# Kernel optimization log

Measured on AMD Instinct MI355X. Metric: run time of the kernel, lower is better.

## Reference

```python
import jax, jax.numpy as jnp
import numpy as np
from jax import lax

N_SRC = 2
K_BASES = 8
N_ITER = 5
NMF_EPS = 1e-20
IP_EPS = 1e-20


def setup_inputs() -> dict:
    key = jax.random.key(0)
    kx, kt, kv = jax.random.split(key, 3)
    M, J, I = 2, 2048, 1025
    X = jax.random.normal(kx, (M, J, I, 2), dtype=jnp.float32)
    T0 = jax.random.uniform(kt, (I, K_BASES, N_SRC), dtype=jnp.float32,
                            minval=1e-08, maxval=1.0)
    V0 = jax.random.uniform(kv, (K_BASES, J, N_SRC), dtype=jnp.float32,
                            minval=1e-08, maxval=1.0)
    return {"X": X, "T0": T0, "V0": V0}


def _nmf_update(Tn, Vn, Yn, eps):
    # Tn: (I,K), Vn: (K,J), Yn: (I,J) complex
    Rn = Tn @ Vn
    magR = jnp.abs(Rn)
    YdR = jnp.abs(Yn) ** 2 / (magR ** 2 + eps)   # |Y|^2 / R^2
    Rd = 1.0 / (magR + eps)
    Tn = Tn * jnp.sqrt((YdR @ Vn.T) / (Rd @ Vn.T + eps))
    Rn = Tn @ Vn
    Rd2 = 1.0 / (jnp.abs(Rn) + eps)
    Vn = Vn * jnp.sqrt((Tn.T @ YdR) / (Tn.T @ Rd2 + eps))
    return Tn, Vn, Tn @ Vn


def _ilrma(X, T0, V0):
    M, J, I, _ = X.shape
    N = N_SRC
    # view_as_complex(X.permute(2,0,1,3)) -> (I, M, J) complex
    Xc = (X[..., 0] + 1j * X[..., 1]).astype(jnp.complex64).transpose(2, 0, 1)
    eye_M = jnp.eye(M, dtype=jnp.complex64)
    W0 = jnp.broadcast_to(jnp.eye(N, M, dtype=jnp.complex64), (I, N, M))
    Y0 = jnp.einsum('inm,imj->inj', W0, Xc)

    def one_iter(carry, _):
        W, T, V, Y = carry
        for n in range(N):  # N=2, structurally distinct small loop
            Tn, Vn, Rn = _nmf_update(T[:, :, n], V[:, :, n], Y[:, n, :], NMF_EPS)
            T = T.at[:, :, n].set(Tn)
            V = V.at[:, :, n].set(Vn)
            # batched per-frequency-bin IP update (vectorizes torch's loop over i)
            inv_Rn = 1.0 / (Rn + IP_EPS)                      # (I,J)
            Xw = Xc * jnp.sqrt(inv_Rn)[:, None, :]            # (I,M,J)
            D = jnp.einsum('imj,ikj->imk', Xw, Xw.conj()) / J  # (I,M,M)
            Dreg = D + IP_EPS * eye_M
            A = jnp.einsum('inm,imk->ink', W, Dreg)           # (I,N,M), N==M
            e_n = eye_M[:, n]                                  # (M,)
            b = jnp.linalg.solve(A, jnp.broadcast_to(e_n, (I, M))[..., None])[..., 0]  # (I,M)
            Db = jnp.einsum('imk,ik->im', Dreg, b)
            denom = jnp.sqrt(jnp.real(jnp.einsum('im,im->i', b.conj(), Db)) + IP_EPS)
            W = W.at[:, n, :].set((b / denom[:, None]).conj())
        Y = jnp.einsum('inm,imj->inj', W, Xc)
        return (W, T, V, Y), None

    (W, T, V, Y), _ = lax.scan(one_iter, (W0, T0, V0, Y0), None, length=N_ITER)
    out = Y.transpose(1, 2, 0)                 # (N, J, I)
    return jnp.stack([out.real, out.imag], axis=-1)  # view_as_real -> (N,J,I,2)


def reference(X, T0, V0):
    return _ilrma(X, T0, V0)
```

## Files before the change

kernel.cpp:

```cpp
#include <hip/hip_runtime.h>

#define I_DIM 1025
#define J_DIM 2048
#define K_B 8
#define IC 33
#define EPSF 1e-20f


__device__ __forceinline__ int rev4i(int x) {
  return ((x & 1) << 3) | ((x & 2) << 1) | ((x & 4) >> 1) | ((x & 8) >> 3);
}
__device__ __forceinline__ int rev3i(int x) {
  return ((x & 1) << 2) | (x & 2) | ((x & 4) >> 2);
}

__device__ __forceinline__ void foldReduce16(float* vals, int lane) {
  #pragma unroll
  for (int step = 0; step < 4; ++step) {
    const int nv = 8 >> step;
    const int bit = (lane >> step) & 1;
    #pragma unroll
    for (int q = 0; q < nv; ++q) {
      float a = vals[q], b = vals[q + nv];
      float send = bit ? a : b;
      float keep = bit ? b : a;
      vals[q] = keep + __shfl_xor(send, 1 << step);
    }
  }
  vals[0] += __shfl_xor(vals[0], 16);
  vals[0] += __shfl_xor(vals[0], 32);
}

__device__ __forceinline__ void foldReduce8(float* vals, int lane) {
  #pragma unroll
  for (int step = 0; step < 3; ++step) {
    const int nv = 4 >> step;
    const int bit = (lane >> step) & 1;
    #pragma unroll
    for (int q = 0; q < nv; ++q) {
      float a = vals[q], b = vals[q + nv];
      float send = bit ? a : b;
      float keep = bit ? b : a;
      vals[q] = keep + __shfl_xor(send, 1 << step);
    }
  }
  vals[0] += __shfl_xor(vals[0], 8);
  vals[0] += __shfl_xor(vals[0], 16);
  vals[0] += __shfl_xor(vals[0], 32);
}

__device__ __forceinline__ float2 cmul(float2 a, float2 b) {
  return make_float2(a.x*b.x - a.y*b.y, a.x*b.y + a.y*b.x);
}
__device__ __forceinline__ float2 cadd(float2 a, float2 b) {
  return make_float2(a.x + b.x, a.y + b.y);
}
__device__ __forceinline__ float2 csub(float2 a, float2 b) {
  return make_float2(a.x - b.x, a.y - b.y);
}
__device__ __forceinline__ float2 cdiv(float2 a, float2 b) {
  float s = 1.0f / (b.x*b.x + b.y*b.y);
  return make_float2((a.x*b.x + a.y*b.y)*s, (a.y*b.x - a.x*b.y)*s);
}

__global__ __launch_bounds__(256) void k_tr_init(
    const float* __restrict__ X, float4* __restrict__ Xq,
    const float* __restrict__ T0, const float* __restrict__ V0,
    float* __restrict__ T, float* __restrict__ V, float* __restrict__ W)
{
  const int tx = threadIdx.x, ty = threadIdx.y;
  const int lt = ty * 32 + tx;
  const int bid = blockIdx.y * 33 + blockIdx.x;
  int t = bid * 256 + lt;
  if (t < 2 * K_B * J_DIM) {
    int n = t >> 14;
    int r = t & 16383;
    int j = r >> 3, k = r & 7;
    V[t] = V0[(k * J_DIM + j) * 2 + n];
  }
  if (t < 2 * I_DIM * K_B) {
    int n = t / (I_DIM * K_B);
    int r = t % (I_DIM * K_B);
    int i = r / K_B, k = r % K_B;
    T[t] = T0[(i * K_B + k) * 2 + n];
  }
  if (t < I_DIM * 8) {
    int u = t & 7;
    int c = u & 1, m = (u >> 1) & 1, n = u >> 2;
    W[t] = (n == m && c == 0) ? 1.0f : 0.0f;
  }
  __shared__ float t0r[32][33], t0i[32][33], t1r[32][33], t1i[32][33];
  const int i0 = blockIdx.x * 32, j0 = blockIdx.y * 32;
  const float2* __restrict__ X2 = (const float2*)X;
  #pragma unroll
  for (int jj = 0; jj < 4; ++jj) {
    int jl = ty + jj * 8;
    int i = i0 + tx;
    if (i < I_DIM) {
      float2 v0 = X2[(size_t)(0 * J_DIM + j0 + jl) * I_DIM + i];
      float2 v1 = X2[(size_t)(1 * J_DIM + j0 + jl) * I_DIM + i];
      t0r[jl][tx] = v0.x; t0i[jl][tx] = v0.y;
      t1r[jl][tx] = v1.x; t1i[jl][tx] = v1.y;
    }
  }
  __syncthreads();
  #pragma unroll
  for (int ii = 0; ii < 4; ++ii) {
    int il = ty + ii * 8;
    int i = i0 + il;
    if (i < I_DIM) {
      Xq[(size_t)i * J_DIM + j0 + tx] =
        make_float4(t0r[tx][il], t0i[tx][il], t1r[tx][il], t1i[tx][il]);
    }
  }
}

template<int N>
__device__ __forceinline__ void nmfT_body(
    int i, int tid,
    const float4* __restrict__ Xq,
    float* __restrict__ T, const float* __restrict__ V,
    const float* __restrict__ W, float* __restrict__ YdR)
{
  float4 xs[8];
  #pragma unroll
  for (int u = 0; u < 8; ++u) xs[u] = Xq[(size_t)i * J_DIM + u * 256 + tid];

  const float4 w = ((const float4*)W)[i * 2 + N];
  float t[K_B];
  const int trow = (N * I_DIM + i) * K_B;
  #pragma unroll
  for (int k = 0; k < K_B; ++k) t[k] = T[trow + k];

  float num[K_B], den[K_B];
  #pragma unroll
  for (int k = 0; k < K_B; ++k) { num[k] = 0.f; den[k] = 0.f; }

  const float4* __restrict__ V4 = (const float4*)V;
  #pragma unroll
  for (int u = 0; u < 8; ++u) {
    int j = u * 256 + tid;
    float4 va = V4[(N * J_DIM + j) * 2 + 0];
    float4 vb = V4[(N * J_DIM + j) * 2 + 1];
    float v[K_B] = {va.x, va.y, va.z, va.w, vb.x, vb.y, vb.z, vb.w};
    float rn = 0.f;
    #pragma unroll
    for (int k = 0; k < K_B; ++k) rn += t[k] * v[k];
    float4 x = xs[u];
    float yr = w.x * x.x - w.y * x.y + w.z * x.z - w.w * x.w;
    float yi = w.x * x.y + w.y * x.x + w.z * x.w + w.w * x.z;
    float rd = 1.0f / (fabsf(rn) + EPSF);
    float ydr = (yr * yr + yi * yi) * rd * rd;
    YdR[(size_t)i * J_DIM + j] = ydr;
    #pragma unroll
    for (int k = 0; k < K_B; ++k) { num[k] += ydr * v[k]; den[k] += rd * v[k]; }
  }

  float vals[16];
  #pragma unroll
  for (int k = 0; k < K_B; ++k) { vals[k] = num[k]; vals[K_B + k] = den[k]; }
  const int wave = tid >> 6, lane = tid & 63;
  foldReduce16(vals, lane);
  __shared__ float redT[4][16];
  if (lane < 16) redT[wave][lane] = vals[0];
  __syncthreads();
  if (tid < K_B) {
    int r = rev4i(tid);
    float nm = redT[0][r] + redT[1][r] + redT[2][r] + redT[3][r];
    float dn = redT[0][r+1] + redT[1][r+1] + redT[2][r+1] + redT[3][r+1];
    T[trow + tid] *= sqrtf(nm / (dn + EPSF));
  }
}

__device__ __forceinline__ void ip_solve_both(
    int i,
    float D000, float p0, float q0, float D110,
    float D001, float p1, float q1, float D111,
    float* __restrict__ W)
{
  float4 w0 = ((const float4*)W)[i * 2 + 0];
  float4 w1 = ((const float4*)W)[i * 2 + 1];
  float2 W00 = make_float2(w0.x, w0.y), W01 = make_float2(w0.z, w0.w);
  float2 W10 = make_float2(w1.x, w1.y), W11 = make_float2(w1.z, w1.w);
  {
    float D00 = D000 + EPSF, D11 = D110 + EPSF;
    float2 D01 = make_float2(p0, q0);
    float2 D10 = make_float2(p0, -q0);
    float2 A00 = cadd(make_float2(W00.x * D00, W00.y * D00), cmul(W01, D10));
    float2 A01 = cadd(cmul(W00, D01), make_float2(W01.x * D11, W01.y * D11));
    float2 A10 = cadd(make_float2(W10.x * D00, W10.y * D00), cmul(W11, D10));
    float2 A11 = cadd(cmul(W10, D01), make_float2(W11.x * D11, W11.y * D11));
    float2 det = csub(cmul(A00, A11), cmul(A01, A10));
    float2 b0 = cdiv(A11, det);
    float2 b1 = cdiv(make_float2(-A10.x, -A10.y), det);
    float2 Db0 = cadd(make_float2(D00 * b0.x, D00 * b0.y), cmul(D01, b1));
    float2 Db1 = cadd(cmul(D10, b0), make_float2(D11 * b1.x, D11 * b1.y));
    float ip = b0.x * Db0.x + b0.y * Db0.y + b1.x * Db1.x + b1.y * Db1.y;
    float inv = 1.0f / sqrtf(ip + EPSF);
    W00 = make_float2(b0.x * inv, -b0.y * inv);
    W01 = make_float2(b1.x * inv, -b1.y * inv);
  }
  {
    float D00 = D001 + EPSF, D11 = D111 + EPSF;
    float2 D01 = make_float2(p1, q1);
    float2 D10 = make_float2(p1, -q1);
    float2 A00 = cadd(make_float2(W00.x * D00, W00.y * D00), cmul(W01, D10));
    float2 A01 = cadd(cmul(W00, D01), make_float2(W01.x * D11, W01.y * D11));
    float2 A10 = cadd(make_float2(W10.x * D00, W10.y * D00), cmul(W11, D10));
    float2 A11 = cadd(cmul(W10, D01), make_float2(W11.x * D11, W11.y * D11));
    float2 det = csub(cmul(A00, A11), cmul(A01, A10));
    float2 b0 = cdiv(make_float2(-A01.x, -A01.y), det);
    float2 b1 = cdiv(A00, det);
    float2 Db0 = cadd(make_float2(D00 * b0.x, D00 * b0.y), cmul(D01, b1));
    float2 Db1 = cadd(cmul(D10, b0), make_float2(D11 * b1.x, D11 * b1.y));
    float ip = b0.x * Db0.x + b0.y * Db0.y + b1.x * Db1.x + b1.y * Db1.y;
    float inv = 1.0f / sqrtf(ip + EPSF);
    W10 = make_float2(b0.x * inv, -b0.y * inv);
    W11 = make_float2(b1.x * inv, -b1.y * inv);
  }
  ((float4*)W)[i * 2 + 0] = make_float4(W00.x, W00.y, W01.x, W01.y);
  ((float4*)W)[i * 2 + 1] = make_float4(W10.x, W10.y, W11.x, W11.y);
}

template<int N>
__device__ __forceinline__ void part_body(
    int pb, int tid,
    const float* __restrict__ T, const float* __restrict__ V,
    const float* __restrict__ YdR,
    float* __restrict__ Pn, float* __restrict__ Pd)
{
  const int jb = pb & 7;
  const int c  = pb >> 3;
  const int j  = jb * 256 + tid;
  const int i0 = c * 32;
  const int ni = min(32, I_DIM - i0);
  __shared__ float sT[32 * K_B];
  if (tid < ni * K_B) sT[tid] = T[(N * I_DIM + i0) * K_B + tid];
  __syncthreads();
  const float4* __restrict__ V4 = (const float4*)V;
  float4 va = V4[(N * J_DIM + j) * 2 + 0];
  float4 vb = V4[(N * J_DIM + j) * 2 + 1];
  float v[K_B] = {va.x, va.y, va.z, va.w, vb.x, vb.y, vb.z, vb.w};
  float num[K_B], den[K_B];
  #pragma unroll
  for (int k = 0; k < K_B; ++k) { num[k] = 0.f; den[k] = 0.f; }

  if (ni == 32) {
    #pragma unroll
    for (int g = 0; g < 4; ++g) {
      float yd[8];
      #pragma unroll
      for (int q = 0; q < 8; ++q)
        yd[q] = YdR[(size_t)(i0 + g * 8 + q) * J_DIM + j];
      #pragma unroll
      for (int q = 0; q < 8; ++q) {
        const int ii = g * 8 + q;
        float rn = 0.f;
        #pragma unroll
        for (int k = 0; k < K_B; ++k) rn += sT[ii * K_B + k] * v[k];
        float rd2 = 1.0f / (fabsf(rn) + EPSF);
        #pragma unroll
        for (int k = 0; k < K_B; ++k) {
          num[k] += sT[ii * K_B + k] * yd[q];
          den[k] += sT[ii * K_B + k] * rd2;
        }
      }
    }
  } else {
    for (int ii = 0; ii < ni; ++ii) {
      float ydr = YdR[(size_t)(i0 + ii) * J_DIM + j];
      float rn = 0.f;
      #pragma unroll
      for (int k = 0; k < K_B; ++k) rn += sT[ii * K_B + k] * v[k];
      float rd2 = 1.0f / (fabsf(rn) + EPSF);
      #pragma unroll
      for (int k = 0; k < K_B; ++k) {
        num[k] += sT[ii * K_B + k] * ydr;
        den[k] += sT[ii * K_B + k] * rd2;
      }
    }
  }
  ((float4*)Pn)[((size_t)c * J_DIM + j) * 2 + 0] = make_float4(num[0], num[1], num[2], num[3]);
  ((float4*)Pn)[((size_t)c * J_DIM + j) * 2 + 1] = make_float4(num[4], num[5], num[6], num[7]);
  ((float4*)Pd)[((size_t)c * J_DIM + j) * 2 + 0] = make_float4(den[0], den[1], den[2], den[3]);
  ((float4*)Pd)[((size_t)c * J_DIM + j) * 2 + 1] = make_float4(den[4], den[5], den[6], den[7]);
}

template<int N>
__device__ __forceinline__ void fin_body(
    int fb, int tid, float* __restrict__ V,
    const float* __restrict__ Pn, const float* __restrict__ Pd)
{
  const int t = fb * 256 + tid;
  float nm = 0.f, dn = 0.f;
  #pragma unroll
  for (int c = 0; c < IC; ++c) {
    nm += Pn[(size_t)c * (K_B * J_DIM) + t];
    dn += Pd[(size_t)c * (K_B * J_DIM) + t];
  }
  V[N * (K_B * J_DIM) + t] *= sqrtf(nm / (dn + EPSF));
}

__global__ __launch_bounds__(256) void k_nmf2(
    const float4* __restrict__ Xq, float* __restrict__ T,
    const float* __restrict__ V, const float* __restrict__ W,
    float* __restrict__ YdR0, float* __restrict__ YdR1)
{
  int b = blockIdx.x;
  int p, pop;
  if (b >= 2048) { p = 1024; pop = b - 2048; }
  else { pop = (b >> 3) & 1; p = ((b >> 4) << 3) | (b & 7); }
  if (pop == 0)
    nmfT_body<0>(p, threadIdx.x, Xq, T, V, W, YdR0);
  else
    nmfT_body<1>(p, threadIdx.x, Xq, T, V, W, YdR1);
}

__global__ __launch_bounds__(256) void k_part2(
    const float* __restrict__ T, const float* __restrict__ V,
    const float* __restrict__ Y0, const float* __restrict__ Y1,
    float* __restrict__ Pn0, float* __restrict__ Pd0,
    float* __restrict__ Pn1, float* __restrict__ Pd1)
{
  if (blockIdx.x < 264)
    part_body<0>(blockIdx.x, threadIdx.x, T, V, Y0, Pn0, Pd0);
  else
    part_body<1>(blockIdx.x - 264, threadIdx.x, T, V, Y1, Pn1, Pd1);
}

__global__ __launch_bounds__(256) void k_fin2(
    float* __restrict__ V,
    const float* __restrict__ Pn0, const float* __restrict__ Pd0,
    const float* __restrict__ Pn1, const float* __restrict__ Pd1)
{
  if (blockIdx.x < 64)
    fin_body<0>(blockIdx.x, threadIdx.x, V, Pn0, Pd0);
  else
    fin_body<1>(blockIdx.x - 64, threadIdx.x, V, Pn1, Pd1);
}

__global__ __launch_bounds__(256) void k_ip2(
    const float4* __restrict__ Xq, const float* __restrict__ T,
    const float* __restrict__ V, float* __restrict__ W)
{
  const int i = blockIdx.x;
  const int tid = threadIdx.x;
  float4 xs[8];
  #pragma unroll
  for (int u = 0; u < 8; ++u) xs[u] = Xq[(size_t)i * J_DIM + u * 256 + tid];

  float t0[K_B], t1[K_B];
  #pragma unroll
  for (int k = 0; k < K_B; ++k) {
    t0[k] = T[(0 * I_DIM + i) * K_B + k];
    t1[k] = T[(1 * I_DIM + i) * K_B + k];
  }
  const float4* __restrict__ V4 = (const float4*)V;
  float acc[8];
  #pragma unroll
  for (int q = 0; q < 8; ++q) acc[q] = 0.f;

  #pragma unroll
  for (int u = 0; u < 8; ++u) {
    int j = u * 256 + tid;
    float4 va0 = V4[(0 * J_DIM + j) * 2 + 0];
    float4 vb0 = V4[(0 * J_DIM + j) * 2 + 1];
    float4 va1 = V4[(1 * J_DIM + j) * 2 + 0];
    float4 vb1 = V4[(1 * J_DIM + j) * 2 + 1];
    float rn0 = t0[0]*va0.x + t0[1]*va0.y + t0[2]*va0.z + t0[3]*va0.w
              + t0[4]*vb0.x + t0[5]*vb0.y + t0[6]*vb0.z + t0[7]*vb0.w;
    float rn1 = t1[0]*va1.x + t1[1]*va1.y + t1[2]*va1.z + t1[3]*va1.w
              + t1[4]*vb1.x + t1[5]*vb1.y + t1[6]*vb1.z + t1[7]*vb1.w;
    float w0 = 1.0f / (rn0 + EPSF);
    float w1 = 1.0f / (rn1 + EPSF);
    float4 x = xs[u];
    float m00 = x.x * x.x + x.y * x.y;
    float m11 = x.z * x.z + x.w * x.w;
    float m01r = x.x * x.z + x.y * x.w;
    float m01i = x.y * x.z - x.x * x.w;
    acc[0] += m00 * w0; acc[1] += m01r * w0; acc[2] += m01i * w0; acc[3] += m11 * w0;
    acc[4] += m00 * w1; acc[5] += m01r * w1; acc[6] += m01i * w1; acc[7] += m11 * w1;
  }
  const int wave = tid >> 6, lane = tid & 63;
  foldReduce8(acc, lane);
  __shared__ float red[4][8];
  if (lane < 8) red[wave][lane] = acc[0];
  __syncthreads();
  if (tid == 0) {
    const float invJ = 1.0f / (float)J_DIM;
    float s[8];
    #pragma unroll
    for (int vv = 0; vv < 8; ++vv) {
      int r = rev3i(vv);
      s[vv] = (red[0][r] + red[1][r] + red[2][r] + red[3][r]) * invJ;
    }
    ip_solve_both(i, s[0], s[1], s[2], s[3], s[4], s[5], s[6], s[7], W);
  }
}

__global__ __launch_bounds__(256) void k_out(
    const float* __restrict__ X, const float* __restrict__ W, float* __restrict__ out)
{
  const int j = blockIdx.x;
  const int i = blockIdx.y * 256 + threadIdx.x;
  if (i >= I_DIM) return;
  const float2* __restrict__ X2 = (const float2*)X;
  float2 x0 = X2[(size_t)(0 * J_DIM + j) * I_DIM + i];
  float2 x1 = X2[(size_t)(1 * J_DIM + j) * I_DIM + i];
  const float4* __restrict__ W4 = (const float4*)W;
  float4 w0 = W4[i * 2 + 0];
  float4 w1 = W4[i * 2 + 1];
  float2* __restrict__ O = (float2*)out;
  float yr = w0.x * x0.x - w0.y * x0.y + w0.z * x1.x - w0.w * x1.y;
  float yi = w0.x * x0.y + w0.y * x0.x + w0.z * x1.y + w0.w * x1.x;
  O[(size_t)(0 * J_DIM + j) * I_DIM + i] = make_float2(yr, yi);
  yr = w1.x * x0.x - w1.y * x0.y + w1.z * x1.x - w1.w * x1.y;
  yi = w1.x * x0.y + w1.y * x0.x + w1.z * x1.y + w1.w * x1.x;
  O[(size_t)(1 * J_DIM + j) * I_DIM + i] = make_float2(yr, yi);
}

extern "C" void kernel_launch(void* const* d_in, const int* in_sizes, int n_in,
                              void* d_out, int out_size, void* d_ws, size_t ws_size,
                              hipStream_t stream) {
  const float* X  = (const float*)d_in[0];
  const float* T0 = (const float*)d_in[1];
  const float* V0 = (const float*)d_in[2];
  float* ws = (float*)d_ws;
  float4* Xq  = (float4*)ws;
  float* YdR0 = ws + 8396800;
  float* YdR1 = ws + 10496000;
  float* T    = ws + 12595200;
  float* V    = ws + 12611600;
  float* W    = ws + 12644368;
  float* Pn0  = ws + 12652568;
  float* Pd0  = ws + 13193240;
  float* Pn1  = ws + 13733912;
  float* Pd1  = ws + 14274584;
  float* out  = (float*)d_out;

  k_tr_init<<<dim3(33, 64), dim3(32, 8), 0, stream>>>(X, Xq, T0, V0, T, V, W);
  for (int it = 0; it < 5; ++it) {
    k_nmf2<<<2 * I_DIM, 256, 0, stream>>>(Xq, T, V, W, YdR0, YdR1);
    k_part2<<<2 * 264, 256, 0, stream>>>(T, V, YdR0, YdR1, Pn0, Pd0, Pn1, Pd1);
    k_fin2<<<2 * 64, 256, 0, stream>>>(V, Pn0, Pd0, Pn1, Pd1);
    k_ip2<<<I_DIM, 256, 0, stream>>>(Xq, T, V, W);
  }
  k_out<<<dim3(J_DIM, 5), 256, 0, stream>>>(X, W, out);
}
```

Baseline: 292.8 us.

## Fuse ILRMA iterations into one persistent cooperative kernel with grid syncs

Replaces the 21 per-iteration kernel launches with a single cooperative persistent kernel. Its stages (NMF T-update, partial V sums, V finalize, IP update, output) are separated by grid-wide syncs. Each block keeps its X row in LDS so it is reused across iterations. The change also switches divisions to hardware reciprocal intrinsics, vectorizes the V-finalize reduction with float4, and loads T tiles into LDS as float4. The intent is to remove launch overhead and repeated X reads. In exchange the grid is limited to co-resident blocks (two per CU), which lowers latency hiding, and the approximate reciprocal may change precision slightly. The old multi-kernel path remains as a fallback.

Result: slower. 929.5 us (+217.5%).

```diff
diff --git a/kernel.cpp b/kernel.cpp
--- a/kernel.cpp
+++ b/kernel.cpp
@@ -1,10 +1,13 @@
 #include <hip/hip_runtime.h>
+#include <hip/hip_cooperative_groups.h>
 
 #define I_DIM 1025
 #define J_DIM 2048
 #define K_B 8
 #define IC 33
 #define EPSF 1e-20f
+
+namespace cg = cooperative_groups;
 
 
 __device__ __forceinline__ int rev4i(int x) {
@@ -116,19 +119,14 @@
 }
 
 template<int N>
-__device__ __forceinline__ void nmfT_body(
-    int i, int tid,
-    const float4* __restrict__ Xq,
+__device__ __forceinline__ void nmfT_src(
+    const float4* xs, int i, int tid,
     float* __restrict__ T, const float* __restrict__ V,
     const float* __restrict__ W, float* __restrict__ YdR)
 {
-  float4 xs[8];
-  #pragma unroll
-  for (int u = 0; u < 8; ++u) xs[u] = Xq[(size_t)i * J_DIM + u * 256 + tid];
-
   const float4 w = ((const float4*)W)[i * 2 + N];
+  const int trow = (N * I_DIM + i) * K_B;
   float t[K_B];
-  const int trow = (N * I_DIM + i) * K_B;
   #pragma unroll
   for (int k = 0; k < K_B; ++k) t[k] = T[trow + k];
 
@@ -149,7 +147,7 @@
     float4 x = xs[u];
     float yr = w.x * x.x - w.y * x.y + w.z * x.z - w.w * x.w;
     float yi = w.x * x.y + w.y * x.x + w.z * x.w + w.w * x.z;
-    float rd = 1.0f / (fabsf(rn) + EPSF);
+    float rd = __builtin_amdgcn_rcpf(fabsf(rn) + EPSF);
     float ydr = (yr * yr + yi * yi) * rd * rd;
     YdR[(size_t)i * J_DIM + j] = ydr;
     #pragma unroll
@@ -170,6 +168,18 @@
     float dn = redT[0][r+1] + redT[1][r+1] + redT[2][r+1] + redT[3][r+1];
     T[trow + tid] *= sqrtf(nm / (dn + EPSF));
   }
+}
+
+__device__ __forceinline__ void nmf_pair(
+    const float4* xs, int i, int tid,
+    float* __restrict__ T, const float* __restrict__ V,
+    const float* __restrict__ W,
+    float* __restrict__ Y0, float* __restrict__ Y1)
+{
+  nmfT_src<0>(xs, i, tid, T, V, W, Y0);
+  __syncthreads();
+  nmfT_src<1>(xs, i, tid, T, V, W, Y1);
+  __syncthreads();
 }
 
 __device__ __forceinline__ void ip_solve_both(
@@ -222,25 +232,87 @@
   ((float4*)W)[i * 2 + 1] = make_float4(W10.x, W10.y, W11.x, W11.y);
 }
 
-template<int N>
-__device__ __forceinline__ void part_body(
-    int pb, int tid,
+__device__ __forceinline__ void ip_pair(
+    const float4* xs, int i, int tid,
     const float* __restrict__ T, const float* __restrict__ V,
-    const float* __restrict__ YdR,
-    float* __restrict__ Pn, float* __restrict__ Pd)
-{
-  const int jb = pb & 7;
-  const int c  = pb >> 3;
-  const int j  = jb * 256 + tid;
+    float* __restrict__ W)
+{
+  float t0[K_B], t1[K_B];
+  #pragma unroll
+  for (int k = 0; k < K_B; ++k) {
+    t0[k] = T[(0 * I_DIM + i) * K_B + k];
+    t1[k] = T[(1 * I_DIM + i) * K_B + k];
+  }
+  const float4* __restrict__ V4 = (const float4*)V;
+  float acc[8];
+  #pragma unroll
+  for (int q = 0; q < 8; ++q) acc[q] = 0.f;
+
+  #pragma unroll
+  for (int u = 0; u < 8; ++u) {
+    int j = u * 256 + tid;
+    float4 va0 = V4[(0 * J_DIM + j) * 2 + 0];
+    float4 vb0 = V4[(0 * J_DIM + j) * 2 + 1];
+    float4 va1 = V4[(1 * J_DIM + j) * 2 + 0];
+    float4 vb1 = V4[(1 * J_DIM + j) * 2 + 1];
+    float rn0 = t0[0]*va0.x + t0[1]*va0.y + t0[2]*va0.z + t0[3]*va0.w
+              + t0[4]*vb0.x + t0[5]*vb0.y + t0[6]*vb0.z + t0[7]*vb0.w;
+    float rn1 = t1[0]*va1.x + t1[1]*va1.y + t1[2]*va1.z + t1[3]*va1.w
+              + t1[4]*vb1.x + t1[5]*vb1.y + t1[6]*vb1.z + t1[7]*vb1.w;
+    float w0 = __builtin_amdgcn_rcpf(rn0 + EPSF);
+    float w1 = __builtin_amdgcn_rcpf(rn1 + EPSF);
+    float4 x = xs[u];
+    float m00 = x.x * x.x + x.y * x.y;
+    float m11 = x.z * x.z + x.w * x.w;
+    float m01r = x.x * x.z + x.y * x.w;
+    float m01i = x.y * x.z - x.x * x.w;
+    acc[0] += m00 * w0; acc[1] += m01r * w0; acc[2] += m01i * w0; acc[3] += m11 * w0;
+    acc[4] += m00 * w1; acc[5] += m01r * w1; acc[6] += m01i * w1; acc[7] += m11 * w1;
+  }
+  const int wave = tid >> 6, lane = tid & 63;
+  foldReduce8(acc, lane);
+  __shared__ float redI[4][8];
+  if (lane < 8) redI[wave][lane] = acc[0];
+  __syncthreads();
+  if (tid == 0) {
+    const float invJ = 1.0f / (float)J_DIM;
+    float s[8];
+    #pragma unroll
+    for (int vv = 0; vv < 8; ++vv) {
+      int r = rev3i(vv);
+      s[vv] = (redI[0][r] + redI[1][r] + redI[2][r] + redI[3][r]) * invJ;
+    }
+    ip_solve_both(i, s[0], s[1], s[2], s[3], s[4], s[5], s[6], s[7], W);
+  }
+  __syncthreads();
+}
+
+__device__ __forceinline__ void part_stage(
+    int vb, int tid,
+    const float* __restrict__ T, const float* __restrict__ V,
+    const float* __restrict__ Y0, const float* __restrict__ Y1,
+    float* __restrict__ Pn0, float* __restrict__ Pd0,
+    float* __restrict__ Pn1, float* __restrict__ Pd1)
+{
+  __shared__ float4 sT4[64];
+  __syncthreads();
+  const int src = vb / 264;
+  const int pb = vb % 264;
+  const int jb = pb & 7, c = pb >> 3;
   const int i0 = c * 32;
   const int ni = min(32, I_DIM - i0);
-  __shared__ float sT[32 * K_B];
-  if (tid < ni * K_B) sT[tid] = T[(N * I_DIM + i0) * K_B + tid];
-  __syncthreads();
+  if (tid < ni * 2)
+    sT4[tid] = ((const float4*)(T + (size_t)(src * I_DIM + i0) * K_B))[tid];
+  __syncthreads();
+
+  const float* __restrict__ YdR = src ? Y1 : Y0;
+  float* __restrict__ Pn = src ? Pn1 : Pn0;
+  float* __restrict__ Pd = src ? Pd1 : Pd0;
+  const int j = jb * 256 + tid;
   const float4* __restrict__ V4 = (const float4*)V;
-  float4 va = V4[(N * J_DIM + j) * 2 + 0];
-  float4 vb = V4[(N * J_DIM + j) * 2 + 1];
-  float v[K_B] = {va.x, va.y, va.z, va.w, vb.x, vb.y, vb.z, vb.w};
+  float4 va = V4[(src * J_DIM + j) * 2 + 0];
+  float4 vb4 = V4[(src * J_DIM + j) * 2 + 1];
+  float v[K_B] = {va.x, va.y, va.z, va.w, vb4.x, vb4.y, vb4.z, vb4.w};
   float num[K_B], den[K_B];
   #pragma unroll
   for (int k = 0; k < K_B; ++k) { num[k] = 0.f; den[k] = 0.f; }
@@ -255,28 +327,32 @@
       #pragma unroll
       for (int q = 0; q < 8; ++q) {
         const int ii = g * 8 + q;
+        float4 ta = sT4[ii * 2], tb = sT4[ii * 2 + 1];
+        float tk[K_B] = {ta.x, ta.y, ta.z, ta.w, tb.x, tb.y, tb.z, tb.w};
         float rn = 0.f;
         #pragma unroll
-        for (int k = 0; k < K_B; ++k) rn += sT[ii * K_B + k] * v[k];
-        float rd2 = 1.0f / (fabsf(rn) + EPSF);
+        for (int k = 0; k < K_B; ++k) rn += tk[k] * v[k];
+        float rd2 = __builtin_amdgcn_rcpf(fabsf(rn) + EPSF);
         #pragma unroll
         for (int k = 0; k < K_B; ++k) {
-          num[k] += sT[ii * K_B + k] * yd[q];
-          den[k] += sT[ii * K_B + k] * rd2;
+          num[k] += tk[k] * yd[q];
+          den[k] += tk[k] * rd2;
         }
       }
     }
   } else {
     for (int ii = 0; ii < ni; ++ii) {
       float ydr = YdR[(size_t)(i0 + ii) * J_DIM + j];
+      float4 ta = sT4[ii * 2], tb = sT4[ii * 2 + 1];
+      float tk[K_B] = {ta.x, ta.y, ta.z, ta.w, tb.x, tb.y, tb.z, tb.w};
       float rn = 0.f;
       #pragma unroll
-      for (int k = 0; k < K_B; ++k) rn += sT[ii * K_B + k] * v[k];
-      float rd2 = 1.0f / (fabsf(rn) + EPSF);
+      for (int k = 0; k < K_B; ++k) rn += tk[k] * v[k];
+      float rd2 = __builtin_amdgcn_rcpf(fabsf(rn) + EPSF);
       #pragma unroll
       for (int k = 0; k < K_B; ++k) {
-        num[k] += sT[ii * K_B + k] * ydr;
-        den[k] += sT[ii * K_B + k] * rd2;
+        num[k] += tk[k] * ydr;
+        den[k] += tk[k] * rd2;
       }
     }
   }
@@ -286,34 +362,51 @@
   ((float4*)Pd)[((size_t)c * J_DIM + j) * 2 + 1] = make_float4(den[4], den[5], den[6], den[7]);
 }
 
-template<int N>
-__device__ __forceinline__ void fin_body(
-    int fb, int tid, float* __restrict__ V,
-    const float* __restrict__ Pn, const float* __restrict__ Pd)
-{
-  const int t = fb * 256 + tid;
-  float nm = 0.f, dn = 0.f;
+__device__ __forceinline__ void fin_stage(
+    int vb, int tid, float* __restrict__ V,
+    const float* __restrict__ Pn0, const float* __restrict__ Pd0,
+    const float* __restrict__ Pn1, const float* __restrict__ Pd1)
+{
+  const int src = vb >> 4, fb = vb & 15;
+  const float* __restrict__ Pn = src ? Pn1 : Pn0;
+  const float* __restrict__ Pd = src ? Pd1 : Pd0;
+  const int t4 = fb * 256 + tid;
+  const float4* __restrict__ Pn4 = (const float4*)Pn;
+  const float4* __restrict__ Pd4 = (const float4*)Pd;
+  float4 nm = make_float4(0.f, 0.f, 0.f, 0.f);
+  float4 dn = make_float4(0.f, 0.f, 0.f, 0.f);
   #pragma unroll
   for (int c = 0; c < IC; ++c) {
-    nm += Pn[(size_t)c * (K_B * J_DIM) + t];
-    dn += Pd[(size_t)c * (K_B * J_DIM) + t];
-  }
-  V[N * (K_B * J_DIM) + t] *= sqrtf(nm / (dn + EPSF));
+    float4 a = Pn4[(size_t)c * 4096 + t4];
+    float4 bb = Pd4[(size_t)c * 4096 + t4];
+    nm.x += a.x; nm.y += a.y; nm.z += a.z; nm.w += a.w;
+    dn.x += bb.x; dn.y += bb.y; dn.z += bb.z; dn.w += bb.w;
+  }
+  float4* __restrict__ V4o = (float4*)(V + src * (K_B * J_DIM));
+  float4 v = V4o[t4];
+  v.x *= sqrtf(nm.x / (dn.x + EPSF));
+  v.y *= sqrtf(nm.y / (dn.y + EPSF));
+  v.z *= sqrtf(nm.z / (dn.z + EPSF));
+  v.w *= sqrtf(nm.w / (dn.w + EPSF));
+  V4o[t4] = v;
 }
 
 __global__ __launch_bounds__(256) void k_nmf2(
     const float4* __restrict__ Xq, float* __restrict__ T,
     const float* __restrict__ V, const float* __restrict__ W,
-    float* __restrict__ YdR0, float* __restrict__ YdR1)
+    float* __restrict__ Y0, float* __restrict__ Y1)
 {
   int b = blockIdx.x;
   int p, pop;
   if (b >= 2048) { p = 1024; pop = b - 2048; }
   else { pop = (b >> 3) & 1; p = ((b >> 4) << 3) | (b & 7); }
+  float4 xs[8];
+  #pragma unroll
+  for (int u = 0; u < 8; ++u) xs[u] = Xq[(size_t)p * J_DIM + u * 256 + threadIdx.x];
   if (pop == 0)
-    nmfT_body<0>(p, threadIdx.x, Xq, T, V, W, YdR0);
+    nmfT_src<0>(xs, p, threadIdx.x, T, V, W, Y0);
   else
-    nmfT_body<1>(p, threadIdx.x, Xq, T, V, W, YdR1);
+    nmfT_src<1>(xs, p, threadIdx.x, T, V, W, Y1);
 }
 
 __global__ __launch_bounds__(256) void k_part2(
@@ -322,10 +415,7 @@
     float* __restrict__ Pn0, float* __restrict__ Pd0,
     float* __restrict__ Pn1, float* __restrict__ Pd1)
 {
-  if (blockIdx.x < 264)
-    part_body<0>(blockIdx.x, threadIdx.x, T, V, Y0, Pn0, Pd0);
-  else
-    part_body<1>(blockIdx.x - 264, threadIdx.x, T, V, Y1, Pn1, Pd1);
+  part_stage(blockIdx.x, threadIdx.x, T, V, Y0, Y1, Pn0, Pd0, Pn1, Pd1);
 }
 
 __global__ __launch_bounds__(256) void k_fin2(
@@ -333,69 +423,18 @@
     const float* __restrict__ Pn0, const float* __restrict__ Pd0,
     const float* __restrict__ Pn1, const float* __restrict__ Pd1)
 {
-  if (blockIdx.x < 64)
-    fin_body<0>(blockIdx.x, threadIdx.x, V, Pn0, Pd0);
-  else
-    fin_body<1>(blockIdx.x - 64, threadIdx.x, V, Pn1, Pd1);
+  fin_stage(blockIdx.x, threadIdx.x, V, Pn0, Pd0, Pn1, Pd1);
 }
 
 __global__ __launch_bounds__(256) void k_ip2(
     const float4* __restrict__ Xq, const float* __restrict__ T,
     const float* __restrict__ V, float* __restrict__ W)
 {
-  const int i = blockIdx.x;
-  const int tid = threadIdx.x;
   float4 xs[8];
   #pragma unroll
-  for (int u = 0; u < 8; ++u) xs[u] = Xq[(size_t)i * J_DIM + u * 256 + tid];
-
-  float t0[K_B], t1[K_B];
-  #pragma unroll
-  for (int k = 0; k < K_B; ++k) {
-    t0[k] = T[(0 * I_DIM + i) * K_B + k];
-    t1[k] = T[(1 * I_DIM + i) * K_B + k];
-  }
-  const float4* __restrict__ V4 = (const float4*)V;
-  float acc[8];
-  #pragma unroll
-  for (int q = 0; q < 8; ++q) acc[q] = 0.f;
-
-  #pragma unroll
-  for (int u = 0; u < 8; ++u) {
-    int j = u * 256 + tid;
-    float4 va0 = V4[(0 * J_DIM + j) * 2 + 0];
-    float4 vb0 = V4[(0 * J_DIM + j) * 2 + 1];
-    float4 va1 = V4[(1 * J_DIM + j) * 2 + 0];
-    float4 vb1 = V4[(1 * J_DIM + j) * 2 + 1];
-    float rn0 = t0[0]*va0.x + t0[1]*va0.y + t0[2]*va0.z + t0[3]*va0.w
-              + t0[4]*vb0.x + t0[5]*vb0.y + t0[6]*vb0.z + t0[7]*vb0.w;
-    float rn1 = t1[0]*va1.x + t1[1]*va1.y + t1[2]*va1.z + t1[3]*va1.w
-              + t1[4]*vb1.x + t1[5]*vb1.y + t1[6]*vb1.z + t1[7]*vb1.w;
-    float w0 = 1.0f / (rn0 + EPSF);
-    float w1 = 1.0f / (rn1 + EPSF);
-    float4 x = xs[u];
-    float m00 = x.x * x.x + x.y * x.y;
-    float m11 = x.z * x.z + x.w * x.w;
-    float m01r = x.x * x.z + x.y * x.w;
-    float m01i = x.y * x.z - x.x * x.w;
-    acc[0] += m00 * w0; acc[1] += m01r * w0; acc[2] += m01i * w0; acc[3] += m11 * w0;
-    acc[4] += m00 * w1; acc[5] += m01r * w1; acc[6] += m01i * w1; acc[7] += m11 * w1;
-  }
-  const int wave = tid >> 6, lane = tid & 63;
-  foldReduce8(acc, lane);
-  __shared__ float red[4][8];
-  if (lane < 8) red[wave][lane] = acc[0];
-  __syncthreads();
-  if (tid == 0) {
-    const float invJ = 1.0f / (float)J_DIM;
-    float s[8];
-    #pragma unroll
-    for (int vv = 0; vv < 8; ++vv) {
-      int r = rev3i(vv);
-      s[vv] = (red[0][r] + red[1][r] + red[2][r] + red[3][r]) * invJ;
-    }
-    ip_solve_both(i, s[0], s[1], s[2], s[3], s[4], s[5], s[6], s[7], W);
-  }
+  for (int u = 0; u < 8; ++u)
+    xs[u] = Xq[(size_t)blockIdx.x * J_DIM + u * 256 + threadIdx.x];
+  ip_pair(xs, blockIdx.x, threadIdx.x, T, V, W);
 }
 
 __global__ __launch_bounds__(256) void k_out(
@@ -419,6 +458,78 @@
   O[(size_t)(1 * J_DIM + j) * I_DIM + i] = make_float2(yr, yi);
 }
 
+__global__ void __launch_bounds__(256, 2) k_mega(
+    const float4* __restrict__ Xq, const float* __restrict__ X,
+    float* __restrict__ T, float* __restrict__ V, float* __restrict__ W,
+    float* __restrict__ Y0, float* __restrict__ Y1,
+    float* __restrict__ Pn0, float* __restrict__ Pd0,
+    float* __restrict__ Pn1, float* __restrict__ Pd1,
+    float* __restrict__ out)
+{
+  extern __shared__ float4 Xl[];
+  cg::grid_group gg = cg::this_grid();
+  const int b = blockIdx.x;
+  const int tid = threadIdx.x;
+  const int G = gridDim.x;
+
+  #pragma unroll
+  for (int u = 0; u < 8; ++u)
+    Xl[u * 256 + tid] = Xq[(size_t)b * J_DIM + u * 256 + tid];
+
+  for (int it = 0; it < 5; ++it) {
+    for (int r = b; r < I_DIM; r += G) {
+      float4 xs[8];
+      if (r == b) {
+        #pragma unroll
+        for (int u = 0; u < 8; ++u) xs[u] = Xl[u * 256 + tid];
+      } else {
+        #pragma unroll
+        for (int u = 0; u < 8; ++u) xs[u] = Xq[(size_t)r * J_DIM + u * 256 + tid];
+      }
+      nmf_pair(xs, r, tid, T, V, W, Y0, Y1);
+    }
+    gg.sync();
+    for (int vb = b; vb < 528; vb += G)
+      part_stage(vb, tid, T, V, Y0, Y1, Pn0, Pd0, Pn1, Pd1);
+    gg.sync();
+    for (int vb = b; vb < 32; vb += G)
+      fin_stage(vb, tid, V, Pn0, Pd0, Pn1, Pd1);
+    gg.sync();
+    for (int r = b; r < I_DIM; r += G) {
+      float4 xs[8];
+      if (r == b) {
+        #pragma unroll
+        for (int u = 0; u < 8; ++u) xs[u] = Xl[u * 256 + tid];
+      } else {
+        #pragma unroll
+        for (int u = 0; u < 8; ++u) xs[u] = Xq[(size_t)r * J_DIM + u * 256 + tid];
+      }
+      ip_pair(xs, r, tid, T, V, W);
+    }
+    gg.sync();
+  }
+
+  const float2* __restrict__ X2 = (const float2*)X;
+  const float4* __restrict__ W4 = (const float4*)W;
+  float2* __restrict__ O = (float2*)out;
+  for (int vb = b; vb < 10240; vb += G) {
+    int j = vb & 2047, iseg = vb >> 11;
+    int i = iseg * 256 + tid;
+    if (i < I_DIM) {
+      float2 x0 = X2[(size_t)(0 * J_DIM + j) * I_DIM + i];
+      float2 x1 = X2[(size_t)(1 * J_DIM + j) * I_DIM + i];
+      float4 w0 = W4[i * 2 + 0];
+      float4 w1 = W4[i * 2 + 1];
+      float yr = w0.x * x0.x - w0.y * x0.y + w0.z * x1.x - w0.w * x1.y;
+      float yi = w0.x * x0.y + w0.y * x0.x + w0.z * x1.y + w0.w * x1.x;
+      O[(size_t)(0 * J_DIM + j) * I_DIM + i] = make_float2(yr, yi);
+      yr = w1.x * x0.x - w1.y * x0.y + w1.z * x1.x - w1.w * x1.y;
+      yi = w1.x * x0.y + w1.y * x0.x + w1.z * x1.y + w1.w * x1.x;
+      O[(size_t)(1 * J_DIM + j) * I_DIM + i] = make_float2(yr, yi);
+    }
+  }
+}
+
 extern "C" void kernel_launch(void* const* d_in, const int* in_sizes, int n_in,
                               void* d_out, int out_size, void* d_ws, size_t ws_size,
                               hipStream_t stream) {
@@ -427,8 +538,8 @@
   const float* V0 = (const float*)d_in[2];
   float* ws = (float*)d_ws;
   float4* Xq  = (float4*)ws;
-  float* YdR0 = ws + 8396800;
-  float* YdR1 = ws + 10496000;
+  float* Y0   = ws + 8396800;
+  float* Y1   = ws + 10496000;
   float* T    = ws + 12595200;
   float* V    = ws + 12611600;
   float* W    = ws + 12644368;
@@ -436,14 +547,35 @@
   float* Pd0  = ws + 13193240;
   float* Pn1  = ws + 13733912;
   float* Pd1  = ws + 14274584;
-  float* out  = (float*)d_out;
+  float* outp = (float*)d_out;
 
   k_tr_init<<<dim3(33, 64), dim3(32, 8), 0, stream>>>(X, Xq, T0, V0, T, V, W);
-  for (int it = 0; it < 5; ++it) {
-    k_nmf2<<<2 * I_DIM, 256, 0, stream>>>(Xq, T, V, W, YdR0, YdR1);
-    k_part2<<<2 * 264, 256, 0, stream>>>(T, V, YdR0, YdR1, Pn0, Pd0, Pn1, Pd1);
-    k_fin2<<<2 * 64, 256, 0, stream>>>(V, Pn0, Pd0, Pn1, Pd1);
-    k_ip2<<<I_DIM, 256, 0, stream>>>(Xq, T, V, W);
-  }
-  k_out<<<dim3(J_DIM, 5), 256, 0, stream>>>(X, W, out);
-}
+
+  bool mega_ok = false;
+  int occ = 0;
+  hipError_t qerr = hipOccupancyMaxActiveBlocksPerMultiprocessor(
+      &occ, k_mega, 256, (size_t)32768);
+  if (qerr == hipSuccess && occ > 0) {
+    int grid = occ * 256;
+    if (grid > 1024) grid = 1024;
+    void* args[] = {(void*)&Xq, (void*)&X, (void*)&T, (void*)&V, (void*)&W,
+                    (void*)&Y0, (void*)&Y1, (void*)&Pn0, (void*)&Pd0,
+                    (void*)&Pn1, (void*)&Pd1, (void*)&outp};
+    hipError_t lerr = hipLaunchCooperativeKernel(
+        (const void*)k_mega, dim3(grid), dim3(256), args, 32768, stream);
+    mega_ok = (lerr == hipSuccess);
+    if (!mega_ok) (void)hipGetLastError();
+  } else {
+    (void)hipGetLastError();
+  }
+
+  if (!mega_ok) {
+    for (int it = 0; it < 5; ++it) {
+      k_nmf2<<<2 * I_DIM, 256, 0, stream>>>(Xq, T, V, W, Y0, Y1);
+      k_part2<<<528, 256, 0, stream>>>(T, V, Y0, Y1, Pn0, Pd0, Pn1, Pd1);
+      k_fin2<<<32, 256, 0, stream>>>(V, Pn0, Pd0, Pn1, Pd1);
+      k_ip2<<<I_DIM, 256, 0, stream>>>(Xq, T, V, W);
+    }
+    k_out<<<dim3(J_DIM, 5), 256, 0, stream>>>(X, W, outp);
+  }
+}
```

## Split V and partials into planar float4 halves and use fast reciprocal

Applied to the files above, without the earlier changes.

Changes the V layout from interleaved [n][j][k] to [n][half][j][4], so each float4 load of V across threads is fully coalesced. The Pn/Pd partial buffers get the same planar layout, and the final reduction kernel now reads and writes float4, running 32 blocks instead of 128. It also swaps exact division for the hardware rcp builtin in the NMF and IP kernels and loads T tiles as float4 from shared memory. The rcp approximation may differ slightly in precision.

After: 276.8 us. 1.06x faster.

```diff
diff --git a/kernel.cpp b/kernel.cpp
--- a/kernel.cpp
+++ b/kernel.cpp
@@ -75,7 +75,10 @@
   if (t < 2 * K_B * J_DIM) {
     int n = t >> 14;
     int r = t & 16383;
-    int j = r >> 3, k = r & 7;
+    int p = r >> 13;
+    int r2 = r & 8191;
+    int j = r2 >> 2, c = r2 & 3;
+    int k = p * 4 + c;
     V[t] = V0[(k * J_DIM + j) * 2 + n];
   }
   if (t < 2 * I_DIM * K_B) {
@@ -116,19 +119,19 @@
 }
 
 template<int N>
-__device__ __forceinline__ void nmfT_body(
+__device__ __forceinline__ void nmfT_src(
     int i, int tid,
-    const float4* __restrict__ Xq,
-    float* __restrict__ T, const float* __restrict__ V,
-    const float* __restrict__ W, float* __restrict__ YdR)
+    const float4* __restrict__ Xq, float* __restrict__ T,
+    const float4* __restrict__ V4, const float* __restrict__ W,
+    float* __restrict__ YdR)
 {
   float4 xs[8];
   #pragma unroll
   for (int u = 0; u < 8; ++u) xs[u] = Xq[(size_t)i * J_DIM + u * 256 + tid];
 
   const float4 w = ((const float4*)W)[i * 2 + N];
+  const int trow = (N * I_DIM + i) * K_B;
   float t[K_B];
-  const int trow = (N * I_DIM + i) * K_B;
   #pragma unroll
   for (int k = 0; k < K_B; ++k) t[k] = T[trow + k];
 
@@ -136,12 +139,11 @@
   #pragma unroll
   for (int k = 0; k < K_B; ++k) { num[k] = 0.f; den[k] = 0.f; }
 
-  const float4* __restrict__ V4 = (const float4*)V;
   #pragma unroll
   for (int u = 0; u < 8; ++u) {
     int j = u * 256 + tid;
-    float4 va = V4[(N * J_DIM + j) * 2 + 0];
-    float4 vb = V4[(N * J_DIM + j) * 2 + 1];
+    float4 va = V4[(N * 2 + 0) * J_DIM + j];
+    float4 vb = V4[(N * 2 + 1) * J_DIM + j];
     float v[K_B] = {va.x, va.y, va.z, va.w, vb.x, vb.y, vb.z, vb.w};
     float rn = 0.f;
     #pragma unroll
@@ -149,7 +151,7 @@
     float4 x = xs[u];
     float yr = w.x * x.x - w.y * x.y + w.z * x.z - w.w * x.w;
     float yi = w.x * x.y + w.y * x.x + w.z * x.w + w.w * x.z;
-    float rd = 1.0f / (fabsf(rn) + EPSF);
+    float rd = __builtin_amdgcn_rcpf(fabsf(rn) + EPSF);
     float ydr = (yr * yr + yi * yi) * rd * rd;
     YdR[(size_t)i * J_DIM + j] = ydr;
     #pragma unroll
@@ -222,25 +224,46 @@
   ((float4*)W)[i * 2 + 1] = make_float4(W10.x, W10.y, W11.x, W11.y);
 }
 
-template<int N>
-__device__ __forceinline__ void part_body(
-    int pb, int tid,
-    const float* __restrict__ T, const float* __restrict__ V,
-    const float* __restrict__ YdR,
-    float* __restrict__ Pn, float* __restrict__ Pd)
-{
-  const int jb = pb & 7;
-  const int c  = pb >> 3;
-  const int j  = jb * 256 + tid;
+__global__ __launch_bounds__(256) void k_nmf2(
+    const float4* __restrict__ Xq, float* __restrict__ T,
+    const float4* __restrict__ V4, const float* __restrict__ W,
+    float* __restrict__ Y0, float* __restrict__ Y1)
+{
+  int b = blockIdx.x;
+  int p, pop;
+  if (b >= 2048) { p = 1024; pop = b - 2048; }
+  else { pop = (b >> 3) & 1; p = ((b >> 4) << 3) | (b & 7); }
+  if (pop == 0)
+    nmfT_src<0>(p, threadIdx.x, Xq, T, V4, W, Y0);
+  else
+    nmfT_src<1>(p, threadIdx.x, Xq, T, V4, W, Y1);
+}
+
+__global__ __launch_bounds__(256) void k_part2(
+    const float* __restrict__ T, const float4* __restrict__ V4,
+    const float* __restrict__ Y0, const float* __restrict__ Y1,
+    float4* __restrict__ Pn0, float4* __restrict__ Pd0,
+    float4* __restrict__ Pn1, float4* __restrict__ Pd1)
+{
+  const int vb = blockIdx.x;
+  const int tid = threadIdx.x;
+  const int src = vb / 264;
+  const int pb = vb % 264;
+  const int jb = pb & 7, c = pb >> 3;
   const int i0 = c * 32;
   const int ni = min(32, I_DIM - i0);
-  __shared__ float sT[32 * K_B];
-  if (tid < ni * K_B) sT[tid] = T[(N * I_DIM + i0) * K_B + tid];
+  __shared__ float4 sT4[64];
+  if (tid < ni * 2)
+    sT4[tid] = ((const float4*)(T + (size_t)(src * I_DIM + i0) * K_B))[tid];
   __syncthreads();
-  const float4* __restrict__ V4 = (const float4*)V;
-  float4 va = V4[(N * J_DIM + j) * 2 + 0];
-  float4 vb = V4[(N * J_DIM + j) * 2 + 1];
-  float v[K_B] = {va.x, va.y, va.z, va.w, vb.x, vb.y, vb.z, vb.w};
+
+  const float* __restrict__ YdR = src ? Y1 : Y0;
+  float4* __restrict__ Pn = src ? Pn1 : Pn0;
+  float4* __restrict__ Pd = src ? Pd1 : Pd0;
+  const int j = jb * 256 + tid;
+  float4 va = V4[(src * 2 + 0) * J_DIM + j];
+  float4 vb4 = V4[(src * 2 + 1) * J_DIM + j];
+  float v[K_B] = {va.x, va.y, va.z, va.w, vb4.x, vb4.y, vb4.z, vb4.w};
   float num[K_B], den[K_B];
   #pragma unroll
   for (int k = 0; k < K_B; ++k) { num[k] = 0.f; den[k] = 0.f; }
@@ -255,93 +278,72 @@
       #pragma unroll
       for (int q = 0; q < 8; ++q) {
         const int ii = g * 8 + q;
+        float4 ta = sT4[ii * 2], tb = sT4[ii * 2 + 1];
+        float tk[K_B] = {ta.x, ta.y, ta.z, ta.w, tb.x, tb.y, tb.z, tb.w};
         float rn = 0.f;
         #pragma unroll
-        for (int k = 0; k < K_B; ++k) rn += sT[ii * K_B + k] * v[k];
-        float rd2 = 1.0f / (fabsf(rn) + EPSF);
+        for (int k = 0; k < K_B; ++k) rn += tk[k] * v[k];
+        float rd2 = __builtin_amdgcn_rcpf(fabsf(rn) + EPSF);
         #pragma unroll
         for (int k = 0; k < K_B; ++k) {
-          num[k] += sT[ii * K_B + k] * yd[q];
-          den[k] += sT[ii * K_B + k] * rd2;
+          num[k] += tk[k] * yd[q];
+          den[k] += tk[k] * rd2;
         }
       }
     }
   } else {
     for (int ii = 0; ii < ni; ++ii) {
       float ydr = YdR[(size_t)(i0 + ii) * J_DIM + j];
+      float4 ta = sT4[ii * 2], tb = sT4[ii * 2 + 1];
+      float tk[K_B] = {ta.x, ta.y, ta.z, ta.w, tb.x, tb.y, tb.z, tb.w};
       float rn = 0.f;
       #pragma unroll
-      for (int k = 0; k < K_B; ++k) rn += sT[ii * K_B + k] * v[k];
-      float rd2 = 1.0f / (fabsf(rn) + EPSF);
+      for (int k = 0; k < K_B; ++k) rn += tk[k] * v[k];
+      float rd2 = __builtin_amdgcn_rcpf(fabsf(rn) + EPSF);
       #pragma unroll
       for (int k = 0; k < K_B; ++k) {
-        num[k] += sT[ii * K_B + k] * ydr;
-        den[k] += sT[ii * K_B + k] * rd2;
+        num[k] += tk[k] * ydr;
+        den[k] += tk[k] * rd2;
       }
     }
   }
-  ((float4*)Pn)[((size_t)c * J_DIM + j) * 2 + 0] = make_float4(num[0], num[1], num[2], num[3]);
-  ((float4*)Pn)[((size_t)c * J_DIM + j) * 2 + 1] = make_float4(num[4], num[5], num[6], num[7]);
-  ((float4*)Pd)[((size_t)c * J_DIM + j) * 2 + 0] = make_float4(den[0], den[1], den[2], den[3]);
-  ((float4*)Pd)[((size_t)c * J_DIM + j) * 2 + 1] = make_float4(den[4], den[5], den[6], den[7]);
-}
-
-template<int N>
-__device__ __forceinline__ void fin_body(
-    int fb, int tid, float* __restrict__ V,
-    const float* __restrict__ Pn, const float* __restrict__ Pd)
-{
-  const int t = fb * 256 + tid;
-  float nm = 0.f, dn = 0.f;
+  Pn[((size_t)c * 2 + 0) * J_DIM + j] = make_float4(num[0], num[1], num[2], num[3]);
+  Pn[((size_t)c * 2 + 1) * J_DIM + j] = make_float4(num[4], num[5], num[6], num[7]);
+  Pd[((size_t)c * 2 + 0) * J_DIM + j] = make_float4(den[0], den[1], den[2], den[3]);
+  Pd[((size_t)c * 2 + 1) * J_DIM + j] = make_float4(den[4], den[5], den[6], den[7]);
+}
+
+__global__ __launch_bounds__(256) void k_fin2(
+    float4* __restrict__ V4,
+    const float4* __restrict__ Pn0, const float4* __restrict__ Pd0,
+    const float4* __restrict__ Pn1, const float4* __restrict__ Pd1)
+{
+  const int vb = blockIdx.x;
+  const int tid = threadIdx.x;
+  const int src = vb >> 4, fb = vb & 15;
+  const float4* __restrict__ Pn = src ? Pn1 : Pn0;
+  const float4* __restrict__ Pd = src ? Pd1 : Pd0;
+  const int t4 = fb * 256 + tid;
+  float4 nm = make_float4(0.f, 0.f, 0.f, 0.f);
+  float4 dn = make_float4(0.f, 0.f, 0.f, 0.f);
   #pragma unroll
   for (int c = 0; c < IC; ++c) {
-    nm += Pn[(size_t)c * (K_B * J_DIM) + t];
-    dn += Pd[(size_t)c * (K_B * J_DIM) + t];
-  }
-  V[N * (K_B * J_DIM) + t] *= sqrtf(nm / (dn + EPSF));
-}
-
-__global__ __launch_bounds__(256) void k_nmf2(
-    const float4* __restrict__ Xq, float* __restrict__ T,
-    const float* __restrict__ V, const float* __restrict__ W,
-    float* __restrict__ YdR0, float* __restrict__ YdR1)
-{
-  int b = blockIdx.x;
-  int p, pop;
-  if (b >= 2048) { p = 1024; pop = b - 2048; }
-  else { pop = (b >> 3) & 1; p = ((b >> 4) << 3) | (b & 7); }
-  if (pop == 0)
-    nmfT_body<0>(p, threadIdx.x, Xq, T, V, W, YdR0);
-  else
-    nmfT_body<1>(p, threadIdx.x, Xq, T, V, W, YdR1);
-}
-
-__global__ __launch_bounds__(256) void k_part2(
-    const float* __restrict__ T, const float* __restrict__ V,
-    const float* __restrict__ Y0, const float* __restrict__ Y1,
-    float* __restrict__ Pn0, float* __restrict__ Pd0,
-    float* __restrict__ Pn1, float* __restrict__ Pd1)
-{
-  if (blockIdx.x < 264)
-    part_body<0>(blockIdx.x, threadIdx.x, T, V, Y0, Pn0, Pd0);
-  else
-    part_body<1>(blockIdx.x - 264, threadIdx.x, T, V, Y1, Pn1, Pd1);
-}
-
-__global__ __launch_bounds__(256) void k_fin2(
-    float* __restrict__ V,
-    const float* __restrict__ Pn0, const float* __restrict__ Pd0,
-    const float* __restrict__ Pn1, const float* __restrict__ Pd1)
-{
-  if (blockIdx.x < 64)
-    fin_body<0>(blockIdx.x, threadIdx.x, V, Pn0, Pd0);
-  else
-    fin_body<1>(blockIdx.x - 64, threadIdx.x, V, Pn1, Pd1);
+    float4 a = Pn[(size_t)c * 4096 + t4];
+    float4 bb = Pd[(size_t)c * 4096 + t4];
+    nm.x += a.x; nm.y += a.y; nm.z += a.z; nm.w += a.w;
+    dn.x += bb.x; dn.y += bb.y; dn.z += bb.z; dn.w += bb.w;
+  }
+  float4 v = V4[src * 4096 + t4];
+  v.x *= sqrtf(nm.x / (dn.x + EPSF));
+  v.y *= sqrtf(nm.y / (dn.y + EPSF));
+  v.z *= sqrtf(nm.z / (dn.z + EPSF));
+  v.w *= sqrtf(nm.w / (dn.w + EPSF));
+  V4[src * 4096 + t4] = v;
 }
 
 __global__ __launch_bounds__(256) void k_ip2(
     const float4* __restrict__ Xq, const float* __restrict__ T,
-    const float* __restrict__ V, float* __restrict__ W)
+    const float4* __restrict__ V4, float* __restrict__ W)
 {
   const int i = blockIdx.x;
   const int tid = threadIdx.x;
@@ -355,7 +357,6 @@
     t0[k] = T[(0 * I_DIM + i) * K_B + k];
     t1[k] = T[(1 * I_DIM + i) * K_B + k];
   }
-  const float4* __restrict__ V4 = (const float4*)V;
   float acc[8];
   #pragma unroll
   for (int q = 0; q < 8; ++q) acc[q] = 0.f;
@@ -363,16 +364,16 @@
   #pragma unroll
   for (int u = 0; u < 8; ++u) {
     int j = u * 256 + tid;
-    float4 va0 = V4[(0 * J_DIM + j) * 2 + 0];
-    float4 vb0 = V4[(0 * J_DIM + j) * 2 + 1];
-    float4 va1 = V4[(1 * J_DIM + j) * 2 + 0];
-    float4 vb1 = V4[(1 * J_DIM + j) * 2 + 1];
+    float4 va0 = V4[0 * J_DIM + j];
+    float4 vb0 = V4[1 * J_DIM + j];
+    float4 va1 = V4[2 * J_DIM + j];
+    float4 vb1 = V4[3 * J_DIM + j];
     float rn0 = t0[0]*va0.x + t0[1]*va0.y + t0[2]*va0.z + t0[3]*va0.w
               + t0[4]*vb0.x + t0[5]*vb0.y + t0[6]*vb0.z + t0[7]*vb0.w;
     float rn1 = t1[0]*va1.x + t1[1]*va1.y + t1[2]*va1.z + t1[3]*va1.w
               + t1[4]*vb1.x + t1[5]*vb1.y + t1[6]*vb1.z + t1[7]*vb1.w;
-    float w0 = 1.0f / (rn0 + EPSF);
-    float w1 = 1.0f / (rn1 + EPSF);
+    float w0 = __builtin_amdgcn_rcpf(rn0 + EPSF);
+    float w1 = __builtin_amdgcn_rcpf(rn1 + EPSF);
     float4 x = xs[u];
     float m00 = x.x * x.x + x.y * x.y;
     float m11 = x.z * x.z + x.w * x.w;
@@ -383,8 +384,8 @@
   }
   const int wave = tid >> 6, lane = tid & 63;
   foldReduce8(acc, lane);
-  __shared__ float red[4][8];
-  if (lane < 8) red[wave][lane] = acc[0];
+  __shared__ float redI[4][8];
+  if (lane < 8) redI[wave][lane] = acc[0];
   __syncthreads();
   if (tid == 0) {
     const float invJ = 1.0f / (float)J_DIM;
@@ -392,7 +393,7 @@
     #pragma unroll
     for (int vv = 0; vv < 8; ++vv) {
       int r = rev3i(vv);
-      s[vv] = (red[0][r] + red[1][r] + red[2][r] + red[3][r]) * invJ;
+      s[vv] = (redI[0][r] + redI[1][r] + redI[2][r] + redI[3][r]) * invJ;
     }
     ip_solve_both(i, s[0], s[1], s[2], s[3], s[4], s[5], s[6], s[7], W);
   }
@@ -427,23 +428,24 @@
   const float* V0 = (const float*)d_in[2];
   float* ws = (float*)d_ws;
   float4* Xq  = (float4*)ws;
-  float* YdR0 = ws + 8396800;
-  float* YdR1 = ws + 10496000;
+  float* Y0   = ws + 8396800;
+  float* Y1   = ws + 10496000;
   float* T    = ws + 12595200;
   float* V    = ws + 12611600;
   float* W    = ws + 12644368;
-  float* Pn0  = ws + 12652568;
-  float* Pd0  = ws + 13193240;
-  float* Pn1  = ws + 13733912;
-  float* Pd1  = ws + 14274584;
-  float* out  = (float*)d_out;
+  float4* Pn0 = (float4*)(ws + 12652568);
+  float4* Pd0 = (float4*)(ws + 13193240);
+  float4* Pn1 = (float4*)(ws + 13733912);
+  float4* Pd1 = (float4*)(ws + 14274584);
+  float4* V4  = (float4*)V;
+  float* outp = (float*)d_out;
 
   k_tr_init<<<dim3(33, 64), dim3(32, 8), 0, stream>>>(X, Xq, T0, V0, T, V, W);
   for (int it = 0; it < 5; ++it) {
-    k_nmf2<<<2 * I_DIM, 256, 0, stream>>>(Xq, T, V, W, YdR0, YdR1);
-    k_part2<<<2 * 264, 256, 0, stream>>>(T, V, YdR0, YdR1, Pn0, Pd0, Pn1, Pd1);
-    k_fin2<<<2 * 64, 256, 0, stream>>>(V, Pn0, Pd0, Pn1, Pd1);
-    k_ip2<<<I_DIM, 256, 0, stream>>>(Xq, T, V, W);
-  }
-  k_out<<<dim3(J_DIM, 5), 256, 0, stream>>>(X, W, out);
-}
+    k_nmf2<<<2 * I_DIM, 256, 0, stream>>>(Xq, T, V4, W, Y0, Y1);
+    k_part2<<<528, 256, 0, stream>>>(T, V4, Y0, Y1, Pn0, Pd0, Pn1, Pd1);
+    k_fin2<<<32, 256, 0, stream>>>(V4, Pn0, Pd0, Pn1, Pd1);
+    k_ip2<<<I_DIM, 256, 0, stream>>>(Xq, T, V4, W);
+  }
+  k_out<<<dim3(J_DIM, 5), 256, 0, stream>>>(X, W, outp);
+}
```
